# Kernel tuning notes

Measured on AMD Instinct MI355X. Metric: run time of the kernel, lower is better.

The kernel has to match this reference:

```python
import jax, jax.numpy as jnp
import numpy as np

NUM_HEADS = 4

def setup_inputs() -> dict:
    key = jax.random.key(0)
    ks = jax.random.split(key, 7)
    B, Lq, Lk, E, D, LAT = 16, 256, 4096, 64, 32, 32
    query = jax.random.normal(ks[0], (B, Lq, E), dtype=jnp.float32)
    key_in = jax.random.normal(ks[1], (B, Lk, E), dtype=jnp.float32)
    value = jax.random.normal(ks[2], (B, Lk, D), dtype=jnp.float32)
    mask = jax.random.randint(ks[3], (B, Lk, D), 0, 2, dtype=jnp.int32)
    Wq = jax.random.normal(ks[4], (E, E), dtype=jnp.float32) / np.sqrt(E).astype(np.float32)
    bq = jnp.zeros((E,), dtype=jnp.float32)
    Wk = jax.random.normal(ks[5], (E, E), dtype=jnp.float32) / np.sqrt(E).astype(np.float32)
    bk = jnp.zeros((E,), dtype=jnp.float32)
    Wo = jax.random.normal(ks[6], (NUM_HEADS * D, LAT), dtype=jnp.float32) / np.sqrt(NUM_HEADS * D).astype(np.float32)
    bo = jnp.zeros((LAT,), dtype=jnp.float32)
    return {"query": query, "key": key_in, "value": value, "mask": mask,
            "Wq": Wq, "bq": bq, "Wk": Wk, "bk": bk, "Wo": Wo, "bo": bo}

def reference(query, key, value, mask, Wq, bq, Wk, bk, Wo, bo):
    B, Lk, D = value.shape
    Lq = query.shape[1]
    h = NUM_HEADS
    ek = query.shape[-1] // h  # embed_time_k
    # linear maps (torch Linear: y = x @ W; here W stored as (in, out))
    q = (query @ Wq + bq).reshape(B, Lq, h, ek).transpose(0, 2, 1, 3)  # (B,h,Lq,ek)
    k = (key @ Wk + bk).reshape(B, Lk, h, ek).transpose(0, 2, 1, 3)    # (B,h,Lk,ek)
    scores = jnp.einsum('bhqe,bhke->bhqk', q, k) / jnp.sqrt(jnp.asarray(ek, q.dtype))
    # Original repeats scores over D, masks per-feature with -inf, softmaxes over Lk,
    # then does a weighted sum. Equivalent fused form (never builds (B,h,Lq,Lk,D)):
    e = jnp.exp(scores - jnp.max(scores, axis=-1, keepdims=True))  # (B,h,Lq,Lk)
    m = mask.astype(value.dtype)                                   # (B,Lk,D) 0/1
    num = jnp.einsum('bhqk,bkd->bhqd', e, m * value)
    den = jnp.einsum('bhqk,bkd->bhqd', e, m)
    x = num / den                                                  # (B,h,Lq,D)
    x = x.transpose(0, 2, 1, 3).reshape(B, Lq, h * D)
    return x @ Wo + bo  # (B, Lq, latent_dim)
```

## Files before the change

### kernel.cpp

```cpp
#include <hip/hip_runtime.h>
#include <hip/hip_bf16.h>
#include <math.h>

typedef __bf16 bf16;
typedef bf16 bf16x4 __attribute__((ext_vector_type(4)));
typedef bf16 bf16x8 __attribute__((ext_vector_type(8)));
typedef float f32x4 __attribute__((ext_vector_type(4)));

#define B_   16
#define LQ_  256
#define LK_  4096
#define E_   64
#define H_   4
#define EK_  16
#define D_   32
#define LAT_ 32

#define OFF_QP    0u
#define OFF_KP    524288u
#define OFF_MVFB  8912896u
#define OFF_WOT   17301504u
#define OFF_NDP   17309696u
#define WS_NEED   50864128u

#define LOG2E 1.44269504f

__device__ inline f32x4 mfma_bf16(bf16x8 a, bf16x8 b, f32x4 c) {
  return __builtin_amdgcn_mfma_f32_16x16x32_bf16(a, b, c, 0, 0, 0);
}
__device__ inline bf16x8 zero8() {
  bf16x8 z;
#pragma unroll
  for (int i = 0; i < 8; ++i) z[i] = (bf16)0.0f;
  return z;
}

__global__ __launch_bounds__(256) void prep_kernel(
    const float* __restrict__ query, const float* __restrict__ key,
    const float* __restrict__ value, const int* __restrict__ mask,
    const float* __restrict__ Wq, const float* __restrict__ bq,
    const float* __restrict__ Wk, const float* __restrict__ bk,
    const float* __restrict__ Wo,
    bf16* __restrict__ qp, bf16* __restrict__ kp,
    bf16* __restrict__ mvfB, bf16* __restrict__ WoT)
{
  __shared__ __align__(16) bf16 s_b[16896];
  const int bid = blockIdx.x;
  const int tid = threadIdx.x;

  if (bid < 544) {
    const bool isQ = bid < 32;
    const int row0 = isQ ? bid * 128 : (bid - 32) * 128;
    const float* in   = isQ ? query : key;
    const float* W    = isQ ? Wq : Wk;
    const float* bias = isQ ? bq : bk;
    bf16* outp        = isQ ? qp : kp;
    const float scal  = isQ ? (0.25f * LOG2E) : 1.0f;

    bf16* sIn = s_b;
    bf16* sWT = s_b + 9216;

#pragma unroll
    for (int p = 0; p < 8; ++p) {
      int f4 = tid + p * 256;
      int row = f4 >> 4, e4 = (f4 & 15) * 4;
      float4 v = *(const float4*)(in + (size_t)(row0 + row) * 64 + e4);
      bf16x4 b4;
      b4[0] = (bf16)v.x; b4[1] = (bf16)v.y; b4[2] = (bf16)v.z; b4[3] = (bf16)v.w;
      *(bf16x4*)(sIn + row * 72 + e4) = b4;
    }
#pragma unroll
    for (int p = 0; p < 4; ++p) {
      int f4 = tid + p * 256;
      int k = f4 >> 4, c4 = (f4 & 15) * 4;
      float4 v = *(const float4*)(W + k * 64 + c4);
      sWT[(c4 + 0) * 72 + k] = (bf16)v.x;
      sWT[(c4 + 1) * 72 + k] = (bf16)v.y;
      sWT[(c4 + 2) * 72 + k] = (bf16)v.z;
      sWT[(c4 + 3) * 72 + k] = (bf16)v.w;
    }
    __syncthreads();

    const int w = tid >> 6, l = tid & 63, l15 = l & 15, g = l >> 4;
    f32x4 acc[2][4];
#pragma unroll
    for (int mt = 0; mt < 2; ++mt)
#pragma unroll
      for (int nt = 0; nt < 4; ++nt) acc[mt][nt] = f32x4{0.f, 0.f, 0.f, 0.f};

#pragma unroll
    for (int ks = 0; ks < 2; ++ks) {
      bf16x8 A0 = *(bf16x8*)(sIn + (32 * w + l15) * 72 + 32 * ks + 8 * g);
      bf16x8 A1 = *(bf16x8*)(sIn + (32 * w + 16 + l15) * 72 + 32 * ks + 8 * g);
#pragma unroll
      for (int nt = 0; nt < 4; ++nt) {
        bf16x8 Bf = *(bf16x8*)(sWT + (16 * nt + l15) * 72 + 32 * ks + 8 * g);
        acc[0][nt] = mfma_bf16(A0, Bf, acc[0][nt]);
        acc[1][nt] = mfma_bf16(A1, Bf, acc[1][nt]);
      }
    }
#pragma unroll
    for (int mt = 0; mt < 2; ++mt)
#pragma unroll
      for (int nt = 0; nt < 4; ++nt) {
        int col = 16 * nt + l15;
        float bv = bias[col];
#pragma unroll
        for (int r = 0; r < 4; ++r) {
          int row = row0 + 32 * w + 16 * mt + 4 * g + r;
          outp[(size_t)row * 64 + col] = (bf16)((acc[mt][nt][r] + bv) * scal);
        }
      }
  } else if (bid < 800) {
    const int rb = bid - 544;
    const int b = rb >> 4, kk0 = (rb & 15) * 256;
#pragma unroll
    for (int p = 0; p < 8; ++p) {
      int f4 = tid + p * 256;
      int kk = f4 >> 3, d4 = (f4 & 7) * 4;
      size_t gi = ((size_t)(b * LK_ + kk0 + kk)) * 32 + d4;
      float4 v = *(const float4*)(value + gi);
      int4   m = *(const int4*)(mask + gi);
      s_b[(d4 + 0) * 264 + kk] = (bf16)(m.x ? v.x : 0.0f);
      s_b[(d4 + 1) * 264 + kk] = (bf16)(m.y ? v.y : 0.0f);
      s_b[(d4 + 2) * 264 + kk] = (bf16)(m.z ? v.z : 0.0f);
      s_b[(d4 + 3) * 264 + kk] = (bf16)(m.w ? v.w : 0.0f);
      s_b[(32 + d4 + 0) * 264 + kk] = (bf16)(float)m.x;
      s_b[(32 + d4 + 1) * 264 + kk] = (bf16)(float)m.y;
      s_b[(32 + d4 + 2) * 264 + kk] = (bf16)(float)m.z;
      s_b[(32 + d4 + 3) * 264 + kk] = (bf16)(float)m.w;
    }
    __syncthreads();
    const int col = tid >> 2, seg = tid & 3;
    const int nt = col >> 4, l15c = col & 15;
#pragma unroll
    for (int w2 = 0; w2 < 8; ++w2) {
      int kkg = seg * 64 + w2 * 8;
      int tile = (kk0 + kkg) >> 5;
      int gq = (kkg >> 3) & 3;
      int lane = 16 * gq + l15c;
      uint4 d = *(uint4*)(s_b + col * 264 + kkg);
      *(uint4*)(mvfB + (size_t)((((b * 128 + tile) * 4 + nt) * 64 + lane)) * 8) = d;
    }
  } else {
#pragma unroll
    for (int p = 0; p < 16; ++p) {
      int f = tid + p * 256;
      int k = f >> 5, n = f & 31;
      WoT[n * 128 + k] = (bf16)Wo[f];
    }
  }
}

__global__ __launch_bounds__(256, 8) void attn_kernel(
    const bf16* __restrict__ qp, const bf16* __restrict__ kp,
    const bf16* __restrict__ mvfB, float* __restrict__ ndp)
{
  __shared__ __align__(16) bf16 s_se[4 * 640];

  const int bid = blockIdx.x;
  const int kc = bid & 7, qt = (bid >> 3) & 15, b = bid >> 7;
  const int tid = threadIdx.x;
  const int h = tid >> 6, l = tid & 63, l15 = l & 15, g = l >> 4;
  const int q0 = qt * 16;
  const int tile0 = kc * 16;

  bf16x8 qB;
  if (l < 32) {
    qB = *(const bf16x8*)(qp + (size_t)((b * LQ_ + q0 + l15) * 64 + h * EK_ + g * 8));
  } else { qB = zero8(); }

  f32x4 acc[4];
#pragma unroll
  for (int nt = 0; nt < 4; ++nt) acc[nt] = f32x4{0.f, 0.f, 0.f, 0.f};

  bf16* se_w = s_se + h * 640;
  const bf16* mvt0 = mvfB + (size_t)(b * 128 + tile0) * 2048;
  const bf16* kp_b = kp + (size_t)(b * LK_ + tile0 * 32) * 64 + h * EK_ + g * 8;

#pragma unroll 2
  for (int t = 0; t < 16; ++t) {
    const bf16* mvt = mvt0 + (size_t)t * 2048;

    bf16x8 mvB[4];
#pragma unroll
    for (int nt = 0; nt < 4; ++nt)
      mvB[nt] = *(const bf16x8*)(mvt + (nt * 64 + l) * 8);

    bf16x8 kA0, kA1;
    if (l < 32) {
      kA0 = *(const bf16x8*)(kp_b + (size_t)(t * 32 + l15) * 64);
      kA1 = *(const bf16x8*)(kp_b + (size_t)(t * 32 + 16 + l15) * 64);
    } else { kA0 = zero8(); kA1 = zero8(); }

    f32x4 S0 = mfma_bf16(kA0, qB, f32x4{0.f, 0.f, 0.f, 0.f});
    f32x4 S1 = mfma_bf16(kA1, qB, f32x4{0.f, 0.f, 0.f, 0.f});

    bf16x4 e0, e1;
#pragma unroll
    for (int r = 0; r < 4; ++r) { e0[r] = (bf16)exp2f(S0[r]); e1[r] = (bf16)exp2f(S1[r]); }
    *(bf16x4*)(se_w + l15 * 40 + 4 * g)      = e0;
    *(bf16x4*)(se_w + l15 * 40 + 16 + 4 * g) = e1;

    asm volatile("" ::: "memory");

    bf16x8 eA = *(bf16x8*)(se_w + l15 * 40 + 8 * g);

#pragma unroll
    for (int nt = 0; nt < 4; ++nt)
      acc[nt] = mfma_bf16(eA, mvB[nt], acc[nt]);
  }

  float* ndp_w = ndp + ((((size_t)kc * B_ + b) * H_ + h) * LQ_) * 64;
#pragma unroll
  for (int nt = 0; nt < 4; ++nt)
#pragma unroll
    for (int r = 0; r < 4; ++r) {
      int q = q0 + 4 * g + r;
      int col = 16 * nt + l15;
      ndp_w[(size_t)q * 64 + col] = acc[nt][r];
    }
}

__global__ __launch_bounds__(256) void out_kernel(
    const float* __restrict__ ndp, const bf16* __restrict__ WoT,
    const float* __restrict__ bo, float* __restrict__ out)
{
  __shared__ __align__(16) bf16 s_x[16 * 136];
  const int bid = blockIdx.x;
  const int b = bid >> 4, q0 = (bid & 15) * 16;
  const int tid = threadIdx.x;
  const int q = tid >> 4, jg = tid & 15;
  const int h = jg >> 2, d0 = (jg & 3) * 8;

  f32x4 nlo = f32x4{0.f,0.f,0.f,0.f}, nhi = f32x4{0.f,0.f,0.f,0.f};
  f32x4 dlo = f32x4{0.f,0.f,0.f,0.f}, dhi = f32x4{0.f,0.f,0.f,0.f};
#pragma unroll
  for (int kc = 0; kc < 8; ++kc) {
    const float* p = ndp + ((((size_t)kc * B_ + b) * H_ + h) * LQ_ + q0 + q) * 64;
    nlo += *(const f32x4*)(p + d0);
    nhi += *(const f32x4*)(p + d0 + 4);
    dlo += *(const f32x4*)(p + 32 + d0);
    dhi += *(const f32x4*)(p + 32 + d0 + 4);
  }
  bf16* sx = s_x + q * 136 + h * 32 + d0;
#pragma unroll
  for (int i = 0; i < 4; ++i) {
    sx[i]     = (bf16)(nlo[i] / dlo[i]);
    sx[4 + i] = (bf16)(nhi[i] / dhi[i]);
  }
  __syncthreads();
  const int w = tid >> 6, l = tid & 63, l15 = l & 15, g = l >> 4;
  if (w < 2) {
    const int nt = w;
    f32x4 acc = f32x4{0.f, 0.f, 0.f, 0.f};
#pragma unroll
    for (int ks = 0; ks < 4; ++ks) {
      bf16x8 A  = *(bf16x8*)(s_x + l15 * 136 + 32 * ks + 8 * g);
      bf16x8 Bf = *(const bf16x8*)(WoT + (l15 + 16 * nt) * 128 + 32 * ks + 8 * g);
      acc = mfma_bf16(A, Bf, acc);
    }
    float bv = bo[l15 + 16 * nt];
#pragma unroll
    for (int r = 0; r < 4; ++r) {
      int row = q0 + 4 * g + r;
      out[(size_t)(b * LQ_ + row) * LAT_ + l15 + 16 * nt] = acc[r] + bv;
    }
  }
}

extern "C" void kernel_launch(void* const* d_in, const int* in_sizes, int n_in,
                              void* d_out, int out_size, void* d_ws, size_t ws_size,
                              hipStream_t stream) {
  const float* query = (const float*)d_in[0];
  const float* key   = (const float*)d_in[1];
  const float* value = (const float*)d_in[2];
  const int*   mask  = (const int*)d_in[3];
  const float* Wq    = (const float*)d_in[4];
  const float* bq    = (const float*)d_in[5];
  const float* Wk    = (const float*)d_in[6];
  const float* bk    = (const float*)d_in[7];
  const float* Wo    = (const float*)d_in[8];
  const float* bo    = (const float*)d_in[9];
  float* out = (float*)d_out;
  char* ws = (char*)d_ws;

  if (ws_size < (size_t)WS_NEED) return;

  bf16* qp   = (bf16*)(ws + OFF_QP);
  bf16* kp   = (bf16*)(ws + OFF_KP);
  bf16* mvfB = (bf16*)(ws + OFF_MVFB);
  bf16* WoT  = (bf16*)(ws + OFF_WOT);
  float* ndp = (float*)(ws + OFF_NDP);

  prep_kernel<<<801, 256, 0, stream>>>(query, key, value, mask, Wq, bq, Wk, bk,
                                       Wo, qp, kp, mvfB, WoT);
  attn_kernel<<<2048, 256, 0, stream>>>(qp, kp, mvfB, ndp);
  out_kernel<<<256, 256, 0, stream>>>(ndp, WoT, bo, out);
}
```

Measured before the change: 140.6 us.

## Process 64 queries per attention block and prefetch next key tile

Each attention block now handles four 16-query tiles instead of one. The key and masked-value fragments loaded from global memory are reused across 64 queries, which cuts redundant global traffic fourfold, and the grid shrinks from 2048 to 512 blocks. Loads for the next key tile are software-prefetched into registers while the current tile is being computed. In exchange the kernel needs more registers and LDS per block, so occupancy drops (launch bounds now allow 2 blocks per CU), and 512 blocks may underfill the GPU's CUs.

```diff
diff --git a/kernel.cpp b/kernel.cpp
--- a/kernel.cpp
+++ b/kernel.cpp
@@ -152,74 +152,103 @@
   }
 }
 
-__global__ __launch_bounds__(256, 8) void attn_kernel(
+__global__ __launch_bounds__(256, 2) void attn_kernel(
     const bf16* __restrict__ qp, const bf16* __restrict__ kp,
     const bf16* __restrict__ mvfB, float* __restrict__ ndp)
 {
-  __shared__ __align__(16) bf16 s_se[4 * 640];
+  __shared__ __align__(16) bf16 s_se[4 * 2560];
 
   const int bid = blockIdx.x;
-  const int kc = bid & 7, qt = (bid >> 3) & 15, b = bid >> 7;
+  const int kc = bid & 7, qt = (bid >> 3) & 3, b = bid >> 5;
   const int tid = threadIdx.x;
   const int h = tid >> 6, l = tid & 63, l15 = l & 15, g = l >> 4;
-  const int q0 = qt * 16;
+  const int q0 = qt * 64;
   const int tile0 = kc * 16;
 
-  bf16x8 qB;
+  bf16x8 qB[4];
   if (l < 32) {
-    qB = *(const bf16x8*)(qp + (size_t)((b * LQ_ + q0 + l15) * 64 + h * EK_ + g * 8));
-  } else { qB = zero8(); }
-
-  f32x4 acc[4];
-#pragma unroll
-  for (int nt = 0; nt < 4; ++nt) acc[nt] = f32x4{0.f, 0.f, 0.f, 0.f};
-
-  bf16* se_w = s_se + h * 640;
+#pragma unroll
+    for (int nt = 0; nt < 4; ++nt)
+      qB[nt] = *(const bf16x8*)(qp + (size_t)((b * LQ_ + q0 + 16 * nt + l15) * 64 + h * EK_ + g * 8));
+  } else {
+#pragma unroll
+    for (int nt = 0; nt < 4; ++nt) qB[nt] = zero8();
+  }
+
+  f32x4 acc[4][4];
+#pragma unroll
+  for (int mq = 0; mq < 4; ++mq)
+#pragma unroll
+    for (int nt = 0; nt < 4; ++nt) acc[mq][nt] = f32x4{0.f, 0.f, 0.f, 0.f};
+
+  bf16* se_w = s_se + h * 2560;
   const bf16* mvt0 = mvfB + (size_t)(b * 128 + tile0) * 2048;
   const bf16* kp_b = kp + (size_t)(b * LK_ + tile0 * 32) * 64 + h * EK_ + g * 8;
 
-#pragma unroll 2
+  bf16x8 mvB[4], kA0, kA1;
+#pragma unroll
+  for (int nt = 0; nt < 4; ++nt)
+    mvB[nt] = *(const bf16x8*)(mvt0 + (nt * 64 + l) * 8);
+  if (l < 32) {
+    kA0 = *(const bf16x8*)(kp_b + (size_t)(l15) * 64);
+    kA1 = *(const bf16x8*)(kp_b + (size_t)(16 + l15) * 64);
+  } else { kA0 = zero8(); kA1 = zero8(); }
+
   for (int t = 0; t < 16; ++t) {
-    const bf16* mvt = mvt0 + (size_t)t * 2048;
-
-    bf16x8 mvB[4];
+    const int tn = (t + 1) & 15;
+    const bf16* mvtn = mvt0 + (size_t)tn * 2048;
+    bf16x8 mvBn[4], kA0n, kA1n;
 #pragma unroll
     for (int nt = 0; nt < 4; ++nt)
-      mvB[nt] = *(const bf16x8*)(mvt + (nt * 64 + l) * 8);
-
-    bf16x8 kA0, kA1;
+      mvBn[nt] = *(const bf16x8*)(mvtn + (nt * 64 + l) * 8);
     if (l < 32) {
-      kA0 = *(const bf16x8*)(kp_b + (size_t)(t * 32 + l15) * 64);
-      kA1 = *(const bf16x8*)(kp_b + (size_t)(t * 32 + 16 + l15) * 64);
-    } else { kA0 = zero8(); kA1 = zero8(); }
-
-    f32x4 S0 = mfma_bf16(kA0, qB, f32x4{0.f, 0.f, 0.f, 0.f});
-    f32x4 S1 = mfma_bf16(kA1, qB, f32x4{0.f, 0.f, 0.f, 0.f});
-
-    bf16x4 e0, e1;
-#pragma unroll
-    for (int r = 0; r < 4; ++r) { e0[r] = (bf16)exp2f(S0[r]); e1[r] = (bf16)exp2f(S1[r]); }
-    *(bf16x4*)(se_w + l15 * 40 + 4 * g)      = e0;
-    *(bf16x4*)(se_w + l15 * 40 + 16 + 4 * g) = e1;
+      kA0n = *(const bf16x8*)(kp_b + (size_t)(tn * 32 + l15) * 64);
+      kA1n = *(const bf16x8*)(kp_b + (size_t)(tn * 32 + 16 + l15) * 64);
+    } else { kA0n = zero8(); kA1n = zero8(); }
+
+    f32x4 S[2][4];
+#pragma unroll
+    for (int nt = 0; nt < 4; ++nt) {
+      S[0][nt] = mfma_bf16(kA0, qB[nt], f32x4{0.f, 0.f, 0.f, 0.f});
+      S[1][nt] = mfma_bf16(kA1, qB[nt], f32x4{0.f, 0.f, 0.f, 0.f});
+    }
+
+#pragma unroll
+    for (int mt = 0; mt < 2; ++mt)
+#pragma unroll
+      for (int nt = 0; nt < 4; ++nt) {
+        bf16x4 e4;
+#pragma unroll
+        for (int r = 0; r < 4; ++r) e4[r] = (bf16)exp2f(S[mt][nt][r]);
+        *(bf16x4*)(se_w + (16 * nt + l15) * 40 + 16 * mt + 4 * g) = e4;
+      }
 
     asm volatile("" ::: "memory");
 
-    bf16x8 eA = *(bf16x8*)(se_w + l15 * 40 + 8 * g);
-
+#pragma unroll
+    for (int mq = 0; mq < 4; ++mq) {
+      bf16x8 eA = *(bf16x8*)(se_w + (16 * mq + l15) * 40 + 8 * g);
+#pragma unroll
+      for (int nt = 0; nt < 4; ++nt)
+        acc[mq][nt] = mfma_bf16(eA, mvB[nt], acc[mq][nt]);
+    }
+
+#pragma unroll
+    for (int nt = 0; nt < 4; ++nt) mvB[nt] = mvBn[nt];
+    kA0 = kA0n; kA1 = kA1n;
+  }
+
+  float* ndp_w = ndp + ((((size_t)kc * B_ + b) * H_ + h) * LQ_) * 64;
+#pragma unroll
+  for (int mq = 0; mq < 4; ++mq)
 #pragma unroll
     for (int nt = 0; nt < 4; ++nt)
-      acc[nt] = mfma_bf16(eA, mvB[nt], acc[nt]);
-  }
-
-  float* ndp_w = ndp + ((((size_t)kc * B_ + b) * H_ + h) * LQ_) * 64;
-#pragma unroll
-  for (int nt = 0; nt < 4; ++nt)
-#pragma unroll
-    for (int r = 0; r < 4; ++r) {
-      int q = q0 + 4 * g + r;
-      int col = 16 * nt + l15;
-      ndp_w[(size_t)q * 64 + col] = acc[nt][r];
-    }
+#pragma unroll
+      for (int r = 0; r < 4; ++r) {
+        int q = q0 + 16 * mq + 4 * g + r;
+        int col = 16 * nt + l15;
+        ndp_w[(size_t)q * 64 + col] = acc[mq][nt][r];
+      }
 }
 
 __global__ __launch_bounds__(256) void out_kernel(
@@ -295,6 +324,6 @@
 
   prep_kernel<<<801, 256, 0, stream>>>(query, key, value, mask, Wq, bq, Wk, bk,
                                        Wo, qp, kp, mvfB, WoT);
-  attn_kernel<<<2048, 256, 0, stream>>>(qp, kp, mvfB, ndp);
+  attn_kernel<<<512, 256, 0, stream>>>(qp, kp, mvfB, ndp);
   out_kernel<<<256, 256, 0, stream>>>(ndp, WoT, bo, out);
 }
```

Result: faster. 131.1 us (-6.7%).
